# Kernel optimization log

Hardware: AMD Instinct MI355X
Metric: run time of the kernel (lower is better)

Reference implementation:

```python
import jax, jax.numpy as jnp
import numpy as np

N, E, D, EDIM = 50000, 800000, 128, 1
LN_EPS = 1e-5
NORM_FACTOR = 1.0


def _ln(x, g, b):
    m = jnp.mean(x, axis=-1, keepdims=True)
    v = jnp.var(x, axis=-1, keepdims=True)
    return (x - m) * jax.lax.rsqrt(v + LN_EPS) * g + b


def _mlp(x, w1, b1, g, be, w2, b2):
    # Linear -> SiLU -> LayerNorm -> Linear (matches nn.Sequential in msg_net/out_net)
    h = jax.nn.silu(x @ w1 + b1)
    h = _ln(h, g, be)
    return h @ w2 + b2


def setup_inputs() -> dict:
    key = jax.random.key(0)
    ks = jax.random.split(key, 24)
    s = 1.0 / np.sqrt(D)
    sa = 1.0 / np.sqrt(2 * D + EDIM)
    f32 = jnp.float32
    return {
        "h": jax.random.normal(ks[0], (N, D), f32),
        "edge_attr": jax.random.uniform(ks[1], (E, EDIM), f32),
        "row": jax.random.randint(ks[2], (E,), 0, N),
        "col": jax.random.randint(ks[3], (E,), 0, N),
        "node_mask": jnp.ones((N, 1), f32),
        "edge_mask": jnp.ones((E, 1), f32),
        "lin_w": jax.random.normal(ks[4], (D, D), f32) * s,
        "lin_b": jnp.zeros((D,), f32),
        "msg_w1": jax.random.normal(ks[5], (D, D), f32) * s,
        "msg_b1": jnp.zeros((D,), f32),
        "msg_ln_g": jnp.ones((D,), f32),
        "msg_ln_b": jnp.zeros((D,), f32),
        "msg_w2": jax.random.normal(ks[6], (D, D), f32) * s,
        "msg_b2": jnp.zeros((D,), f32),
        "att_w1": jax.random.normal(ks[7], (2 * D + EDIM, D), f32) * sa,
        "att_b1": jnp.zeros((D,), f32),
        "att_w2": jax.random.normal(ks[8], (D, 1), f32) * s,
        "att_b2": jnp.zeros((1,), f32),
        "out_w1": jax.random.normal(ks[9], (D, D), f32) * s,
        "out_b1": jnp.zeros((D,), f32),
        "out_ln_g": jnp.ones((D,), f32),
        "out_ln_b": jnp.zeros((D,), f32),
        "out_w2": jax.random.normal(ks[10], (D, D), f32) * s,
        "out_b2": jnp.zeros((D,), f32),
        "ln_g": jnp.ones((D,), f32),
        "ln_b": jnp.zeros((D,), f32),
    }


def reference(h, edge_attr, row, col, node_mask, edge_mask,
              lin_w, lin_b,
              msg_w1, msg_b1, msg_ln_g, msg_ln_b, msg_w2, msg_b2,
              att_w1, att_b1, att_w2, att_b2,
              out_w1, out_b1, out_ln_g, out_ln_b, out_w2, out_b2,
              ln_g, ln_b):
    # h = self.linear(h)
    x = h @ lin_w + lin_b                                    # [N, D]
    # msg_net transform of node features
    x_ = _mlp(x, msg_w1, msg_b1, msg_ln_g, msg_ln_b, msg_w2, msg_b2)
    # DenseAtt: cat(x[row], x[col], edge_attr) -> MLP -> sigmoid -> * edge_mask
    feat = jnp.concatenate([x[row], x[col], edge_attr], axis=1)   # [E, 2D+edge_dim]
    att = jax.nn.sigmoid(jax.nn.silu(feat @ att_w1 + att_b1) @ att_w2 + att_b2)
    att = att * edge_mask                                    # [E, 1]
    # gather -> weighted message -> scatter_add (unsorted_segment_sum, 'sum' norm)
    msg = jax.ops.segment_sum(x_[col] * att, row, num_segments=N) / NORM_FACTOR
    # out_net transform, residual, final LayerNorm
    msg = _mlp(msg, out_w1, out_b1, out_ln_g, out_ln_b, out_w2, out_b2)
    return _ln(x + msg, ln_g, ln_b)                          # [N, D]
```

## Files before the change

### kernel.cpp

```cpp
#include <hip/hip_runtime.h>

#define LN_EPS 1e-5f

typedef __attribute__((ext_vector_type(8))) short short8;
typedef __attribute__((ext_vector_type(4))) float f32x4;

__device__ __forceinline__ float sigf(float x) {
    return __builtin_amdgcn_rcpf(1.0f + __expf(-x));
}

__device__ __forceinline__ unsigned short f2bf(float f) {
    unsigned u = __float_as_uint(f);
    return (unsigned short)((u + 0x7fffu + ((u >> 16) & 1u)) >> 16);
}
__device__ __forceinline__ unsigned f2bf2(float lo, float hi) {
    return (unsigned)f2bf(lo) | ((unsigned)f2bf(hi) << 16);
}
__device__ __forceinline__ void bf2f(unsigned u, float& lo, float& hi) {
    lo = __uint_as_float(u << 16);
    hi = __uint_as_float(u & 0xffff0000u);
}
__device__ __forceinline__ void bf8f(uint4 p, float* o) {
    bf2f(p.x, o[0], o[1]); bf2f(p.y, o[2], o[3]);
    bf2f(p.z, o[4], o[5]); bf2f(p.w, o[6], o[7]);
}
__device__ __forceinline__ float bf1f(unsigned short s) {
    return __uint_as_float(((unsigned)s) << 16);
}

__device__ __forceinline__ float quad_add_all(float x) {
    int v = __builtin_amdgcn_update_dpp(0, __float_as_int(x), 0xB1, 0xF, 0xF, true);
    x += __int_as_float(v);
    v = __builtin_amdgcn_update_dpp(0, __float_as_int(x), 0x4E, 0xF, 0xF, true);
    x += __int_as_float(v);
    return x;
}

__global__ __launch_bounds__(256)
void prep_w(const float* __restrict__ lin_w, const float* __restrict__ msg_w1,
            const float* __restrict__ msg_w2, const float* __restrict__ att_w1,
            const float* __restrict__ out_w1, const float* __restrict__ out_w2,
            const float* __restrict__ att_b1, unsigned short* __restrict__ wp,
            float* __restrict__ bias256)
{
    const int idx = blockIdx.x * 256 + threadIdx.x;
    if (idx < 8 * 16384) {
        const int m = idx >> 14, r = idx & 16383;
        const int k = r >> 7, n = r & 127;
        const float* src; int slot; int fnBase = 0;
        switch (m) {
            case 0: src = lin_w;  slot = 0; break;
            case 1: src = msg_w1; slot = 1; break;
            case 2: src = msg_w2; slot = 2; break;
            case 3: src = att_w1; slot = 3; break;
            case 4: src = att_w1 + 128 * 128; slot = 3; fnBase = 8; break;
            case 5: src = out_w1; slot = 5; break;
            default: src = out_w2; slot = 6; break;
        }
        const float v = src[k * 128 + n];
        const int fn = fnBase + (n >> 4);
        const int fk = k >> 5, kb = (k >> 3) & 3, j = k & 7;
        const size_t dst = (size_t)slot * 16384 + ((size_t)((fn * 4 + fk) * 64 + (n & 15) + 16 * kb)) * 8 + j;
        wp[dst] = f2bf(v);
    } else if (idx < 8 * 16384 + 256) {
        const int t = idx - 8 * 16384;
        bias256[t] = (t < 128) ? att_b1[t] : 0.f;
    }
}

__device__ __forceinline__ short8 ldA_f32(const float* A, size_t row, int k0) {
    const float* ap = A + row * 128 + k0;
    const float4 f0 = *(const float4*)ap;
    const float4 f1 = *(const float4*)(ap + 4);
    union { unsigned u[4]; short8 s; } v;
    v.u[0] = f2bf2(f0.x, f0.y); v.u[1] = f2bf2(f0.z, f0.w);
    v.u[2] = f2bf2(f1.x, f1.y); v.u[3] = f2bf2(f1.z, f1.w);
    return v.s;
}
__device__ __forceinline__ short8 ldA_bf(const unsigned short* A, size_t row, int k0) {
    return *(const short8*)(A + row * 128 + k0);
}

__global__ __launch_bounds__(256, 4)
void front_mfma(const float* __restrict__ h,
                const unsigned short* __restrict__ WpLin, const float* __restrict__ lin_b,
                const unsigned short* __restrict__ WpAtt, const float* __restrict__ bias256,
                const unsigned short* __restrict__ WpM1, const float* __restrict__ msg_b1,
                const float* __restrict__ m1g, const float* __restrict__ m1b,
                const unsigned short* __restrict__ WpM2, const float* __restrict__ msg_b2,
                unsigned short* __restrict__ xbH, unsigned short* __restrict__ xrH,
                unsigned short* __restrict__ xcH, unsigned short* __restrict__ xmH,
                int nrows)
{
    __shared__ unsigned short hofA[4 * 2048];
    __shared__ unsigned short hofB[4 * 2048];
    const int tid = threadIdx.x;
    const int w = tid >> 6, lane = tid & 63;
    const int r0 = blockIdx.x * 64;
    const int arow = r0 + w * 16 + (lane & 15);
    const size_t rowc = (arow < nrows) ? (size_t)arow : (size_t)(nrows - 1);
    const int kh = (lane >> 4) * 8;
    const int cn = lane & 15, rq = lane >> 4;
    unsigned short* hwA = hofA + w * 2048;
    unsigned short* hwB = hofB + w * 2048;

    short8 a[4];
#pragma unroll
    for (int fk = 0; fk < 4; ++fk) a[fk] = ldA_f32(h, rowc, fk * 32 + kh);

    {
        const short8* Bf = (const short8*)WpLin;
        f32x4 accx[8];
#pragma unroll
        for (int fn = 0; fn < 8; ++fn) accx[fn] = (f32x4){0.f, 0.f, 0.f, 0.f};
#pragma unroll
        for (int fk = 0; fk < 4; ++fk)
#pragma unroll
            for (int fn = 0; fn < 8; ++fn)
                accx[fn] = __builtin_amdgcn_mfma_f32_16x16x32_bf16(a[fk], Bf[(fn * 4 + fk) * 64 + lane], accx[fn], 0, 0, 0);

        float bv[8];
#pragma unroll
        for (int fn = 0; fn < 8; ++fn) bv[fn] = lin_b[fn * 16 + cn];
#pragma unroll
        for (int reg = 0; reg < 4; ++reg) {
            const int gr = r0 + w * 16 + rq * 4 + reg;
            const int row16 = rq * 4 + reg;
            const int sw = (row16 & 7) << 3;
#pragma unroll
            for (int fn = 0; fn < 8; ++fn) {
                const unsigned short hb = f2bf(accx[fn][reg] + bv[fn]);
                if (gr < nrows) xbH[(size_t)gr * 128 + fn * 16 + cn] = hb;
                hwA[row16 * 128 + ((fn * 16 + cn) ^ sw)] = hb;
            }
        }
    }

    short8 ax[4];
    {
        const int row16 = lane & 15;
        const int sw = (row16 & 7) << 3;
#pragma unroll
        for (int fk = 0; fk < 4; ++fk)
            ax[fk] = *(const short8*)(hwA + row16 * 128 + ((fk * 32 + kh) ^ sw));
    }

    {
        const short8* Bf = (const short8*)WpAtt;
        f32x4 acca[16];
#pragma unroll
        for (int fn = 0; fn < 16; ++fn) acca[fn] = (f32x4){0.f, 0.f, 0.f, 0.f};
#pragma unroll
        for (int fk = 0; fk < 4; ++fk)
#pragma unroll
            for (int fn = 0; fn < 16; ++fn)
                acca[fn] = __builtin_amdgcn_mfma_f32_16x16x32_bf16(ax[fk], Bf[(fn * 4 + fk) * 64 + lane], acca[fn], 0, 0, 0);

        float bv[16];
#pragma unroll
        for (int fn = 0; fn < 16; ++fn) bv[fn] = bias256[fn * 16 + cn];
#pragma unroll
        for (int reg = 0; reg < 4; ++reg) {
            const int gr = r0 + w * 16 + rq * 4 + reg;
            if (gr < nrows) {
#pragma unroll
                for (int fn = 0; fn < 16; ++fn) {
                    const float v = acca[fn][reg] + bv[fn];
                    if (fn < 8) xrH[(size_t)gr * 128 + fn * 16 + cn] = f2bf(v);
                    else        xcH[(size_t)gr * 128 + (fn - 8) * 16 + cn] = f2bf(v);
                }
            }
        }
    }

    {
        const short8* Bf = (const short8*)WpM1;
        f32x4 acc1[8];
#pragma unroll
        for (int fn = 0; fn < 8; ++fn) acc1[fn] = (f32x4){0.f, 0.f, 0.f, 0.f};
#pragma unroll
        for (int fk = 0; fk < 4; ++fk)
#pragma unroll
            for (int fn = 0; fn < 8; ++fn)
                acc1[fn] = __builtin_amdgcn_mfma_f32_16x16x32_bf16(ax[fk], Bf[(fn * 4 + fk) * 64 + lane], acc1[fn], 0, 0, 0);

        float bv[8], gv[8], bbv[8];
#pragma unroll
        for (int fn = 0; fn < 8; ++fn) {
            bv[fn] = msg_b1[fn * 16 + cn]; gv[fn] = m1g[fn * 16 + cn]; bbv[fn] = m1b[fn * 16 + cn];
        }
#pragma unroll
        for (int reg = 0; reg < 4; ++reg) {
            float val[8];
            float sum = 0.f, sq = 0.f;
#pragma unroll
            for (int fn = 0; fn < 8; ++fn) {
                float v = acc1[fn][reg] + bv[fn];
                v = v * sigf(v);
                val[fn] = v; sum += v; sq += v * v;
            }
#pragma unroll
            for (int m = 1; m < 16; m <<= 1) { sum += __shfl_xor(sum, m); sq += __shfl_xor(sq, m); }
            const float mean = sum * (1.f / 128.f);
            const float var = sq * (1.f / 128.f) - mean * mean;
            const float rstd = rsqrtf(var + LN_EPS);
            const int row16 = rq * 4 + reg;
            const int sw = (row16 & 7) << 3;
#pragma unroll
            for (int fn = 0; fn < 8; ++fn) {
                const float o = (val[fn] - mean) * rstd * gv[fn] + bbv[fn];
                hwB[row16 * 128 + ((fn * 16 + cn) ^ sw)] = f2bf(o);
            }
        }
    }

    short8 am[4];
    {
        const int row16 = lane & 15;
        const int sw = (row16 & 7) << 3;
#pragma unroll
        for (int fk = 0; fk < 4; ++fk)
            am[fk] = *(const short8*)(hwB + row16 * 128 + ((fk * 32 + kh) ^ sw));
    }
    {
        const short8* Bf = (const short8*)WpM2;
        f32x4 acc2[8];
#pragma unroll
        for (int fn = 0; fn < 8; ++fn) acc2[fn] = (f32x4){0.f, 0.f, 0.f, 0.f};
#pragma unroll
        for (int fk = 0; fk < 4; ++fk)
#pragma unroll
            for (int fn = 0; fn < 8; ++fn)
                acc2[fn] = __builtin_amdgcn_mfma_f32_16x16x32_bf16(am[fk], Bf[(fn * 4 + fk) * 64 + lane], acc2[fn], 0, 0, 0);

        float bv[8];
#pragma unroll
        for (int fn = 0; fn < 8; ++fn) bv[fn] = msg_b2[fn * 16 + cn];
#pragma unroll
        for (int reg = 0; reg < 4; ++reg) {
            const int gr = r0 + w * 16 + rq * 4 + reg;
            if (gr < nrows) {
#pragma unroll
                for (int fn = 0; fn < 8; ++fn)
                    xmH[(size_t)gr * 128 + fn * 16 + cn] = f2bf(acc2[fn][reg] + bv[fn]);
            }
        }
    }
}

__global__ __launch_bounds__(256, 4)
void gemm2_mfma(const unsigned short* __restrict__ Av,
                const unsigned short* __restrict__ Wp1, const float* __restrict__ b1,
                const float* __restrict__ ln1g, const float* __restrict__ ln1b,
                const unsigned short* __restrict__ Wp2, const float* __restrict__ b2,
                const float* __restrict__ ln2g, const float* __restrict__ ln2b,
                const unsigned short* __restrict__ resH, float* __restrict__ Cf, int nrows)
{
    __shared__ unsigned short hof[4 * 2048];
    const int tid = threadIdx.x;
    const int w = tid >> 6, lane = tid & 63;
    const int r0 = blockIdx.x * 64;
    const int arow = r0 + w * 16 + (lane & 15);
    const size_t rowc = (arow < nrows) ? (size_t)arow : (size_t)(nrows - 1);
    const int kh = (lane >> 4) * 8;
    const int cn = lane & 15, rq = lane >> 4;

    short8 a[4];
#pragma unroll
    for (int fk = 0; fk < 4; ++fk) a[fk] = ldA_bf(Av, rowc, fk * 32 + kh);

    const short8* B1f = (const short8*)Wp1;
    f32x4 acc[8];
#pragma unroll
    for (int fn = 0; fn < 8; ++fn) acc[fn] = (f32x4){0.f, 0.f, 0.f, 0.f};
#pragma unroll
    for (int fk = 0; fk < 4; ++fk)
#pragma unroll
        for (int fn = 0; fn < 8; ++fn)
            acc[fn] = __builtin_amdgcn_mfma_f32_16x16x32_bf16(a[fk], B1f[(fn * 4 + fk) * 64 + lane], acc[fn], 0, 0, 0);

    unsigned short* hw = hof + w * 2048;
    {
        float bv[8], gv[8], bbv[8];
#pragma unroll
        for (int fn = 0; fn < 8; ++fn) {
            bv[fn] = b1[fn * 16 + cn]; gv[fn] = ln1g[fn * 16 + cn]; bbv[fn] = ln1b[fn * 16 + cn];
        }
#pragma unroll
        for (int reg = 0; reg < 4; ++reg) {
            float val[8];
            float sum = 0.f, sq = 0.f;
#pragma unroll
            for (int fn = 0; fn < 8; ++fn) {
                float v = acc[fn][reg] + bv[fn];
                v = v * sigf(v);
                val[fn] = v; sum += v; sq += v * v;
            }
#pragma unroll
            for (int m = 1; m < 16; m <<= 1) { sum += __shfl_xor(sum, m); sq += __shfl_xor(sq, m); }
            const float mean = sum * (1.f / 128.f);
            const float var = sq * (1.f / 128.f) - mean * mean;
            const float rstd = rsqrtf(var + LN_EPS);
            const int row16 = rq * 4 + reg;
            const int sw = (row16 & 7) << 3;
#pragma unroll
            for (int fn = 0; fn < 8; ++fn) {
                const float o = (val[fn] - mean) * rstd * gv[fn] + bbv[fn];
                hw[row16 * 128 + ((fn * 16 + cn) ^ sw)] = f2bf(o);
            }
        }
    }

    short8 a2[4];
    {
        const int row16 = lane & 15;
        const int sw = (row16 & 7) << 3;
#pragma unroll
        for (int fk = 0; fk < 4; ++fk)
            a2[fk] = *(const short8*)(hw + row16 * 128 + ((fk * 32 + kh) ^ sw));
    }

    const short8* B2f = (const short8*)Wp2;
    f32x4 acc2[8];
#pragma unroll
    for (int fn = 0; fn < 8; ++fn) acc2[fn] = (f32x4){0.f, 0.f, 0.f, 0.f};
#pragma unroll
    for (int fk = 0; fk < 4; ++fk)
#pragma unroll
        for (int fn = 0; fn < 8; ++fn)
            acc2[fn] = __builtin_amdgcn_mfma_f32_16x16x32_bf16(a2[fk], B2f[(fn * 4 + fk) * 64 + lane], acc2[fn], 0, 0, 0);

    float bv2[8], gv[8], bbv[8];
#pragma unroll
    for (int fn = 0; fn < 8; ++fn) {
        bv2[fn] = b2[fn * 16 + cn]; gv[fn] = ln2g[fn * 16 + cn]; bbv[fn] = ln2b[fn * 16 + cn];
    }
#pragma unroll
    for (int reg = 0; reg < 4; ++reg) {
        const int gr = r0 + w * 16 + rq * 4 + reg;
        const int grc = gr < nrows ? gr : nrows - 1;
        float val[8];
        float sum = 0.f, sq = 0.f;
#pragma unroll
        for (int fn = 0; fn < 8; ++fn) {
            float v = acc2[fn][reg] + bv2[fn] + bf1f(resH[(size_t)grc * 128 + fn * 16 + cn]);
            val[fn] = v; sum += v; sq += v * v;
        }
#pragma unroll
        for (int m = 1; m < 16; m <<= 1) { sum += __shfl_xor(sum, m); sq += __shfl_xor(sq, m); }
        const float mean = sum * (1.f / 128.f);
        const float var = sq * (1.f / 128.f) - mean * mean;
        const float rstd = rsqrtf(var + LN_EPS);
        if (gr < nrows) {
#pragma unroll
            for (int fn = 0; fn < 8; ++fn)
                Cf[(size_t)gr * 128 + fn * 16 + cn] = (val[fn] - mean) * rstd * gv[fn] + bbv[fn];
        }
    }
}

__global__ __launch_bounds__(256)
void hist_rank(const int* __restrict__ row, int* __restrict__ cnt,
               int* __restrict__ rank, int E)
{
    const int tid = blockIdx.x * blockDim.x + threadIdx.x;
    const int stride = gridDim.x * blockDim.x;
    for (int e0 = tid; e0 < E; e0 += stride * 8) {
        int r[8]; bool val[8];
#pragma unroll
        for (int u = 0; u < 8; ++u) {
            const int e = e0 + u * stride;
            val[u] = e < E;
            r[u] = val[u] ? row[e] : 0;
        }
        int rk[8];
#pragma unroll
        for (int u = 0; u < 8; ++u)
            if (val[u]) rk[u] = atomicAdd(&cnt[r[u]], 1);
#pragma unroll
        for (int u = 0; u < 8; ++u)
            if (val[u]) rank[e0 + u * stride] = rk[u];
    }
}

__global__ __launch_bounds__(1024)
void scan_a(const int* __restrict__ cnt, int* __restrict__ off,
            int* __restrict__ btot, int n)
{
    __shared__ int wsum[16];
    const int tid = threadIdx.x, lane = tid & 63, wv = tid >> 6;
    const int i = blockIdx.x * 1024 + tid;
    const int v = (i < n) ? cnt[i] : 0;
    int incl = v;
#pragma unroll
    for (int d = 1; d < 64; d <<= 1) { int t = __shfl_up(incl, d); if (lane >= d) incl += t; }
    if (lane == 63) wsum[wv] = incl;
    __syncthreads();
    if (tid == 0) {
        int run = 0;
        for (int ww = 0; ww < 16; ++ww) { int t = wsum[ww]; wsum[ww] = run; run += t; }
    }
    __syncthreads();
    if (i < n) off[i] = wsum[wv] + incl - v;
    if (tid == 1023) btot[blockIdx.x] = wsum[15] + incl;
}

__global__ __launch_bounds__(64)
void scan_b(int* __restrict__ btot, int* __restrict__ bexc,
            int* __restrict__ off, int n, int nb, int E)
{
    const int t = threadIdx.x;
    const int v = (t < nb) ? btot[t] : 0;
    int incl = v;
#pragma unroll
    for (int d = 1; d < 64; d <<= 1) { int u = __shfl_up(incl, d); if (t >= d) incl += u; }
    if (t < nb) bexc[t] = incl - v;
    if (t == 0) off[n] = E;
}

__global__ __launch_bounds__(1024)
void scan_c(int* __restrict__ off, const int* __restrict__ bexc, int n)
{
    const int i = blockIdx.x * 1024 + threadIdx.x;
    if (i < n) off[i] += bexc[blockIdx.x];
}

__global__ __launch_bounds__(256, 4)
void att_edge(const unsigned short* __restrict__ xrH,
              const unsigned short* __restrict__ xcH,
              const int* __restrict__ row, const int* __restrict__ col,
              const float* __restrict__ ea, const float* __restrict__ em,
              const int* __restrict__ rank, const int* __restrict__ off,
              const float* __restrict__ we_, const float* __restrict__ w2_,
              const float* __restrict__ b2p, uint2* __restrict__ catS, int E)
{
    const int lane = threadIdx.x & 63;
    const int q = lane & 3;
    const int gwid = (blockIdx.x * blockDim.x + threadIdx.x) >> 6;
    const int nw = (gridDim.x * blockDim.x) >> 6;

    float we[32], w2[32];
#pragma unroll
    for (int ch = 0; ch < 4; ++ch) {
        const float4 a0 = ((const float4*)we_)[ch * 8 + q * 2];
        const float4 a1 = ((const float4*)we_)[ch * 8 + q * 2 + 1];
        we[ch * 8 + 0] = a0.x; we[ch * 8 + 1] = a0.y; we[ch * 8 + 2] = a0.z; we[ch * 8 + 3] = a0.w;
        we[ch * 8 + 4] = a1.x; we[ch * 8 + 5] = a1.y; we[ch * 8 + 6] = a1.z; we[ch * 8 + 7] = a1.w;
        const float4 c0 = ((const float4*)w2_)[ch * 8 + q * 2];
        const float4 c1 = ((const float4*)w2_)[ch * 8 + q * 2 + 1];
        w2[ch * 8 + 0] = c0.x; w2[ch * 8 + 1] = c0.y; w2[ch * 8 + 2] = c0.z; w2[ch * 8 + 3] = c0.w;
        w2[ch * 8 + 4] = c1.x; w2[ch * 8 + 5] = c1.y; w2[ch * 8 + 6] = c1.z; w2[ch * 8 + 7] = c1.w;
    }
    const float b2 = *b2p;

    for (int base = gwid * 16; base < E; base += nw * 16) {
        const int e = base + (lane >> 2);
        const bool valid = e < E;
        const int ec = valid ? e : E - 1;
        const int r = row[ec], c = col[ec];
        const float eax = ea[ec], emv = em[ec];
        const unsigned short* xr = xrH + (size_t)r * 128;
        const unsigned short* xc = xcH + (size_t)c * 128;
        float pc[4];
#pragma unroll
        for (int ch = 0; ch < 4; ++ch) {
            const uint4 pa = *(const uint4*)(xr + ch * 32 + q * 8);
            const uint4 pb = *(const uint4*)(xc + ch * 32 + q * 8);
            float xa[8], xb[8];
            bf8f(pa, xa); bf8f(pb, xb);
            float s = 0.f;
#pragma unroll
            for (int i = 0; i < 8; ++i) {
                const float t = xa[i] + xb[i] + eax * we[ch * 8 + i];
                s += t * sigf(t) * w2[ch * 8 + i];
            }
            pc[ch] = s;
        }
        float p = (pc[0] + pc[1]) + (pc[2] + pc[3]);
        p = quad_add_all(p);
        const float att = sigf(p + b2) * emv;
        if (valid && q == 0) {
            const int pos = off[r] + rank[ec];
            catS[pos] = make_uint2((unsigned)c, __float_as_uint(att));
        }
    }
}

__global__ __launch_bounds__(256)
void accum_k(const unsigned short* __restrict__ xmH, const int* __restrict__ off,
             const uint2* __restrict__ catS, unsigned short* __restrict__ msgH, int N)
{
    const int lane = threadIdx.x & 63;
    const int g = lane >> 4, l = lane & 15;
    const int gwid = (blockIdx.x * blockDim.x + threadIdx.x) >> 6;
    const int nw = (gridDim.x * blockDim.x) >> 6;
    const uint4* xm4 = (const uint4*)xmH;

    for (int wid = gwid; wid < N; wid += nw) {
        int j0 = off[wid];
        const int jend = off[wid + 1];
        float acc[8] = {0.f, 0.f, 0.f, 0.f, 0.f, 0.f, 0.f, 0.f};

        for (; j0 + 16 <= jend; j0 += 16) {
            uint2 ca[4]; uint4 pk[4];
#pragma unroll
            for (int u = 0; u < 4; ++u) ca[u] = catS[j0 + u * 4 + g];
#pragma unroll
            for (int u = 0; u < 4; ++u) pk[u] = xm4[(size_t)ca[u].x * 16 + l];
#pragma unroll
            for (int u = 0; u < 4; ++u) {
                const float att = __uint_as_float(ca[u].y);
                float xm[8];
                bf8f(pk[u], xm);
#pragma unroll
                for (int i = 0; i < 8; ++i) acc[i] = fmaf(att, xm[i], acc[i]);
            }
        }
        for (; j0 + 8 <= jend; j0 += 8) {
            const uint2 caA = catS[j0 + g];
            const uint2 caB = catS[j0 + 4 + g];
            const uint4 pA = xm4[(size_t)caA.x * 16 + l];
            const uint4 pB = xm4[(size_t)caB.x * 16 + l];
            const float attA = __uint_as_float(caA.y);
            const float attB = __uint_as_float(caB.y);
            float xmA[8], xmB[8];
            bf8f(pA, xmA); bf8f(pB, xmB);
#pragma unroll
            for (int i = 0; i < 8; ++i)
                acc[i] = fmaf(attB, xmB[i], fmaf(attA, xmA[i], acc[i]));
        }
        for (; j0 < jend; j0 += 4) {
            const int je = j0 + g;
            const bool valid = je < jend;
            const int jc = valid ? je : jend - 1;
            const uint2 ca = catS[jc];
            const uint4 p = xm4[(size_t)ca.x * 16 + l];
            const float att = valid ? __uint_as_float(ca.y) : 0.f;
            float xm[8];
            bf8f(p, xm);
#pragma unroll
            for (int i = 0; i < 8; ++i) acc[i] = fmaf(att, xm[i], acc[i]);
        }

#pragma unroll
        for (int i = 0; i < 8; ++i) {
            acc[i] += __shfl_xor(acc[i], 16);
            acc[i] += __shfl_xor(acc[i], 32);
        }
        if (g == 0) {
            uint4 pk;
            pk.x = f2bf2(acc[0], acc[1]); pk.y = f2bf2(acc[2], acc[3]);
            pk.z = f2bf2(acc[4], acc[5]); pk.w = f2bf2(acc[6], acc[7]);
            ((uint4*)msgH)[(size_t)wid * 16 + l] = pk;
        }
    }
}

extern "C" void kernel_launch(void* const* d_in, const int* in_sizes, int n_in,
                              void* d_out, int out_size, void* d_ws, size_t ws_size,
                              hipStream_t stream)
{
    const float* h        = (const float*)d_in[0];
    const float* edge_attr= (const float*)d_in[1];
    const int*   row      = (const int*)d_in[2];
    const int*   col      = (const int*)d_in[3];
    const float* edge_mask= (const float*)d_in[5];
    const float* lin_w    = (const float*)d_in[6];
    const float* lin_b    = (const float*)d_in[7];
    const float* msg_w1   = (const float*)d_in[8];
    const float* msg_b1   = (const float*)d_in[9];
    const float* msg_ln_g = (const float*)d_in[10];
    const float* msg_ln_b = (const float*)d_in[11];
    const float* msg_w2   = (const float*)d_in[12];
    const float* msg_b2   = (const float*)d_in[13];
    const float* att_w1   = (const float*)d_in[14];
    const float* att_b1   = (const float*)d_in[15];
    const float* att_w2   = (const float*)d_in[16];
    const float* att_b2   = (const float*)d_in[17];
    const float* out_w1   = (const float*)d_in[18];
    const float* out_b1   = (const float*)d_in[19];
    const float* out_ln_g = (const float*)d_in[20];
    const float* out_ln_b = (const float*)d_in[21];
    const float* out_w2   = (const float*)d_in[22];
    const float* out_b2   = (const float*)d_in[23];
    const float* ln_g     = (const float*)d_in[24];
    const float* ln_b     = (const float*)d_in[25];

    const int N = in_sizes[0] / 128;
    const int E = in_sizes[2];
    const size_t NF = (size_t)N * 128;

    unsigned short* xbH  = (unsigned short*)d_ws;
    unsigned short* xrH  = xbH + NF;
    unsigned short* xcH  = xrH + NF;
    unsigned short* xmH  = xcH + NF;
    unsigned short* msgH = xmH + NF;
    int*    cnt   = (int*)(msgH + NF);
    int*    off   = cnt + N;
    int*    btot  = off + N + 8;
    int*    bexc  = btot + 64;
    int*    rank  = bexc + 64;
    uint2*  catS  = (uint2*)(rank + E);
    unsigned short* wp = (unsigned short*)(catS + E);
    float* bias256 = (float*)(wp + 8 * 16384);

    const int gb = (N + 63) / 64;
    const int nb = (N + 1023) / 1024;
    const int hgrid = (E + 256 * 8 - 1) / (256 * 8);

    prep_w<<<513, 256, 0, stream>>>(lin_w, msg_w1, msg_w2, att_w1, out_w1, out_w2,
                                    att_b1, wp, bias256);
    hipMemsetAsync(cnt, 0, (size_t)N * sizeof(int), stream);
    hist_rank<<<hgrid, 256, 0, stream>>>(row, cnt, rank, E);
    scan_a<<<nb, 1024, 0, stream>>>(cnt, off, btot, N);
    scan_b<<<1, 64, 0, stream>>>(btot, bexc, off, N, nb, E);
    scan_c<<<nb, 1024, 0, stream>>>(off, bexc, N);

    front_mfma<<<gb, 256, 0, stream>>>(h, wp, lin_b,
                                       wp + 3 * 16384, bias256,
                                       wp + 16384, msg_b1, msg_ln_g, msg_ln_b,
                                       wp + 2 * 16384, msg_b2,
                                       xbH, xrH, xcH, xmH, N);

    att_edge<<<2048, 256, 0, stream>>>(xrH, xcH, row, col, edge_attr, edge_mask,
                                       rank, off, att_w1 + 256 * 128, att_w2, att_b2,
                                       catS, E);

    accum_k<<<2048, 256, 0, stream>>>(xmH, off, catS, msgH, N);

    gemm2_mfma<<<gb, 256, 0, stream>>>(msgH, wp + 5 * 16384, out_b1, out_ln_g, out_ln_b,
                                       wp + 6 * 16384, out_b2, ln_g, ln_b,
                                       xbH, (float*)d_out, N);
}
```

Baseline: 230.9 us.

## Stage front_mfma weights in LDS and coalesce output stores via shared tiles

The front kernel now copies each 128x128 bf16 weight slab into a 32KB shared buffer before its MFMA pass, so B fragments come from LDS instead of repeated global/L2 reads. The fused 256-wide attention GEMM is split into two 128-wide passes. All outputs go through a swizzled LDS tile and are written as 16-byte vector stores rather than scattered 2-byte stores. In exchange the kernel adds several block barriers and more LDS use, and launch bounds drop to 3 blocks per CU.

```diff
diff --git a/kernel.cpp b/kernel.cpp
--- a/kernel.cpp
+++ b/kernel.cpp
@@ -81,19 +81,19 @@
     return *(const short8*)(A + row * 128 + k0);
 }
 
-__global__ __launch_bounds__(256, 4)
+__global__ __launch_bounds__(256, 3)
 void front_mfma(const float* __restrict__ h,
-                const unsigned short* __restrict__ WpLin, const float* __restrict__ lin_b,
-                const unsigned short* __restrict__ WpAtt, const float* __restrict__ bias256,
-                const unsigned short* __restrict__ WpM1, const float* __restrict__ msg_b1,
+                const unsigned short* __restrict__ wp, const float* __restrict__ lin_b,
+                const float* __restrict__ att_b1,
+                const float* __restrict__ msg_b1,
                 const float* __restrict__ m1g, const float* __restrict__ m1b,
-                const unsigned short* __restrict__ WpM2, const float* __restrict__ msg_b2,
+                const float* __restrict__ msg_b2,
                 unsigned short* __restrict__ xbH, unsigned short* __restrict__ xrH,
                 unsigned short* __restrict__ xcH, unsigned short* __restrict__ xmH,
                 int nrows)
 {
-    __shared__ unsigned short hofA[4 * 2048];
-    __shared__ unsigned short hofB[4 * 2048];
+    __shared__ uint4 Bbuf[2048];
+    __shared__ unsigned short hof[4 * 2048];
     const int tid = threadIdx.x;
     const int w = tid >> 6, lane = tid & 63;
     const int r0 = blockIdx.x * 64;
@@ -101,89 +101,93 @@
     const size_t rowc = (arow < nrows) ? (size_t)arow : (size_t)(nrows - 1);
     const int kh = (lane >> 4) * 8;
     const int cn = lane & 15, rq = lane >> 4;
-    unsigned short* hwA = hofA + w * 2048;
-    unsigned short* hwB = hofB + w * 2048;
+    unsigned short* hw = hof + w * 2048;
+    const short8* Bf = (const short8*)Bbuf;
 
     short8 a[4];
 #pragma unroll
     for (int fk = 0; fk < 4; ++fk) a[fk] = ldA_f32(h, rowc, fk * 32 + kh);
 
-    {
-        const short8* Bf = (const short8*)WpLin;
-        f32x4 accx[8];
-#pragma unroll
-        for (int fn = 0; fn < 8; ++fn) accx[fn] = (f32x4){0.f, 0.f, 0.f, 0.f};
-#pragma unroll
-        for (int fk = 0; fk < 4; ++fk)
-#pragma unroll
-            for (int fn = 0; fn < 8; ++fn)
-                accx[fn] = __builtin_amdgcn_mfma_f32_16x16x32_bf16(a[fk], Bf[(fn * 4 + fk) * 64 + lane], accx[fn], 0, 0, 0);
-
+    const uint4* wp4 = (const uint4*)wp;
+
+#define LOADB(slotoff)  { _Pragma("unroll") \
+    for (int i = 0; i < 8; ++i) Bbuf[tid + i * 256] = wp4[(slotoff) + tid + i * 256]; }
+
+#define MFMA8(afrag, accv) { _Pragma("unroll") \
+    for (int fk = 0; fk < 4; ++fk) { _Pragma("unroll") \
+        for (int fn = 0; fn < 8; ++fn) \
+            accv[fn] = __builtin_amdgcn_mfma_f32_16x16x32_bf16(afrag[fk], Bf[(fn * 4 + fk) * 64 + lane], accv[fn], 0, 0, 0); } }
+
+#define EPI_HOF(accv, bvv) { _Pragma("unroll") \
+    for (int reg = 0; reg < 4; ++reg) { \
+        const int row16 = rq * 4 + reg; const int sw = (row16 & 7) << 3; _Pragma("unroll") \
+        for (int fn = 0; fn < 8; ++fn) \
+            hw[row16 * 128 + ((fn * 16 + cn) ^ sw)] = f2bf(accv[fn][reg] + bvv[fn]); } }
+
+#define FLUSH(G) { const int frow = lane >> 2; const int fgr = r0 + w * 16 + frow; \
+    const int fsw = (frow & 7) << 3; _Pragma("unroll") \
+    for (int it = 0; it < 4; ++it) { \
+        const int c0 = ((lane & 3) + it * 4) * 8; \
+        short8 v = *(const short8*)(hw + frow * 128 + (c0 ^ fsw)); \
+        if (fgr < nrows) *(short8*)((G) + (size_t)fgr * 128 + c0) = v; } }
+
+    LOADB(0);
+    __syncthreads();
+    f32x4 acc[8];
+#pragma unroll
+    for (int fn = 0; fn < 8; ++fn) acc[fn] = (f32x4){0.f, 0.f, 0.f, 0.f};
+    MFMA8(a, acc);
+    {
         float bv[8];
 #pragma unroll
         for (int fn = 0; fn < 8; ++fn) bv[fn] = lin_b[fn * 16 + cn];
-#pragma unroll
-        for (int reg = 0; reg < 4; ++reg) {
-            const int gr = r0 + w * 16 + rq * 4 + reg;
-            const int row16 = rq * 4 + reg;
-            const int sw = (row16 & 7) << 3;
-#pragma unroll
-            for (int fn = 0; fn < 8; ++fn) {
-                const unsigned short hb = f2bf(accx[fn][reg] + bv[fn]);
-                if (gr < nrows) xbH[(size_t)gr * 128 + fn * 16 + cn] = hb;
-                hwA[row16 * 128 + ((fn * 16 + cn) ^ sw)] = hb;
-            }
-        }
-    }
-
+        EPI_HOF(acc, bv);
+    }
     short8 ax[4];
     {
         const int row16 = lane & 15;
         const int sw = (row16 & 7) << 3;
 #pragma unroll
         for (int fk = 0; fk < 4; ++fk)
-            ax[fk] = *(const short8*)(hwA + row16 * 128 + ((fk * 32 + kh) ^ sw));
-    }
-
-    {
-        const short8* Bf = (const short8*)WpAtt;
-        f32x4 acca[16];
-#pragma unroll
-        for (int fn = 0; fn < 16; ++fn) acca[fn] = (f32x4){0.f, 0.f, 0.f, 0.f};
-#pragma unroll
-        for (int fk = 0; fk < 4; ++fk)
-#pragma unroll
-            for (int fn = 0; fn < 16; ++fn)
-                acca[fn] = __builtin_amdgcn_mfma_f32_16x16x32_bf16(ax[fk], Bf[(fn * 4 + fk) * 64 + lane], acca[fn], 0, 0, 0);
-
-        float bv[16];
-#pragma unroll
-        for (int fn = 0; fn < 16; ++fn) bv[fn] = bias256[fn * 16 + cn];
-#pragma unroll
-        for (int reg = 0; reg < 4; ++reg) {
-            const int gr = r0 + w * 16 + rq * 4 + reg;
-            if (gr < nrows) {
-#pragma unroll
-                for (int fn = 0; fn < 16; ++fn) {
-                    const float v = acca[fn][reg] + bv[fn];
-                    if (fn < 8) xrH[(size_t)gr * 128 + fn * 16 + cn] = f2bf(v);
-                    else        xcH[(size_t)gr * 128 + (fn - 8) * 16 + cn] = f2bf(v);
-                }
-            }
-        }
-    }
-
-    {
-        const short8* Bf = (const short8*)WpM1;
-        f32x4 acc1[8];
-#pragma unroll
-        for (int fn = 0; fn < 8; ++fn) acc1[fn] = (f32x4){0.f, 0.f, 0.f, 0.f};
-#pragma unroll
-        for (int fk = 0; fk < 4; ++fk)
-#pragma unroll
-            for (int fn = 0; fn < 8; ++fn)
-                acc1[fn] = __builtin_amdgcn_mfma_f32_16x16x32_bf16(ax[fk], Bf[(fn * 4 + fk) * 64 + lane], acc1[fn], 0, 0, 0);
-
+            ax[fk] = *(const short8*)(hw + row16 * 128 + ((fk * 32 + kh) ^ sw));
+    }
+    FLUSH(xbH);
+    __syncthreads();
+
+    LOADB(3 * 2048);
+    __syncthreads();
+#pragma unroll
+    for (int fn = 0; fn < 8; ++fn) acc[fn] = (f32x4){0.f, 0.f, 0.f, 0.f};
+    MFMA8(ax, acc);
+    {
+        float bv[8];
+#pragma unroll
+        for (int fn = 0; fn < 8; ++fn) bv[fn] = att_b1[fn * 16 + cn];
+        EPI_HOF(acc, bv);
+    }
+    FLUSH(xrH);
+    __syncthreads();
+
+    LOADB(4 * 2048);
+    __syncthreads();
+#pragma unroll
+    for (int fn = 0; fn < 8; ++fn) acc[fn] = (f32x4){0.f, 0.f, 0.f, 0.f};
+    MFMA8(ax, acc);
+    {
+        float bv[8];
+#pragma unroll
+        for (int fn = 0; fn < 8; ++fn) bv[fn] = 0.f;
+        EPI_HOF(acc, bv);
+    }
+    FLUSH(xcH);
+    __syncthreads();
+
+    LOADB(1 * 2048);
+    __syncthreads();
+#pragma unroll
+    for (int fn = 0; fn < 8; ++fn) acc[fn] = (f32x4){0.f, 0.f, 0.f, 0.f};
+    MFMA8(ax, acc);
+    {
         float bv[8], gv[8], bbv[8];
 #pragma unroll
         for (int fn = 0; fn < 8; ++fn) {
@@ -195,7 +199,7 @@
             float sum = 0.f, sq = 0.f;
 #pragma unroll
             for (int fn = 0; fn < 8; ++fn) {
-                float v = acc1[fn][reg] + bv[fn];
+                float v = acc[fn][reg] + bv[fn];
                 v = v * sigf(v);
                 val[fn] = v; sum += v; sq += v * v;
             }
@@ -209,43 +213,36 @@
 #pragma unroll
             for (int fn = 0; fn < 8; ++fn) {
                 const float o = (val[fn] - mean) * rstd * gv[fn] + bbv[fn];
-                hwB[row16 * 128 + ((fn * 16 + cn) ^ sw)] = f2bf(o);
+                hw[row16 * 128 + ((fn * 16 + cn) ^ sw)] = f2bf(o);
             }
         }
     }
-
     short8 am[4];
     {
         const int row16 = lane & 15;
         const int sw = (row16 & 7) << 3;
 #pragma unroll
         for (int fk = 0; fk < 4; ++fk)
-            am[fk] = *(const short8*)(hwB + row16 * 128 + ((fk * 32 + kh) ^ sw));
-    }
-    {
-        const short8* Bf = (const short8*)WpM2;
-        f32x4 acc2[8];
-#pragma unroll
-        for (int fn = 0; fn < 8; ++fn) acc2[fn] = (f32x4){0.f, 0.f, 0.f, 0.f};
-#pragma unroll
-        for (int fk = 0; fk < 4; ++fk)
-#pragma unroll
-            for (int fn = 0; fn < 8; ++fn)
-                acc2[fn] = __builtin_amdgcn_mfma_f32_16x16x32_bf16(am[fk], Bf[(fn * 4 + fk) * 64 + lane], acc2[fn], 0, 0, 0);
-
+            am[fk] = *(const short8*)(hw + row16 * 128 + ((fk * 32 + kh) ^ sw));
+    }
+    __syncthreads();
+
+    LOADB(2 * 2048);
+    __syncthreads();
+#pragma unroll
+    for (int fn = 0; fn < 8; ++fn) acc[fn] = (f32x4){0.f, 0.f, 0.f, 0.f};
+    MFMA8(am, acc);
+    {
         float bv[8];
 #pragma unroll
         for (int fn = 0; fn < 8; ++fn) bv[fn] = msg_b2[fn * 16 + cn];
-#pragma unroll
-        for (int reg = 0; reg < 4; ++reg) {
-            const int gr = r0 + w * 16 + rq * 4 + reg;
-            if (gr < nrows) {
-#pragma unroll
-                for (int fn = 0; fn < 8; ++fn)
-                    xmH[(size_t)gr * 128 + fn * 16 + cn] = f2bf(acc2[fn][reg] + bv[fn]);
-            }
-        }
-    }
+        EPI_HOF(acc, bv);
+    }
+    FLUSH(xmH);
+#undef LOADB
+#undef MFMA8
+#undef EPI_HOF
+#undef FLUSH
 }
 
 __global__ __launch_bounds__(256, 4)
@@ -616,10 +613,8 @@
     scan_b<<<1, 64, 0, stream>>>(btot, bexc, off, N, nb, E);
     scan_c<<<nb, 1024, 0, stream>>>(off, bexc, N);
 
-    front_mfma<<<gb, 256, 0, stream>>>(h, wp, lin_b,
-                                       wp + 3 * 16384, bias256,
-                                       wp + 16384, msg_b1, msg_ln_g, msg_ln_b,
-                                       wp + 2 * 16384, msg_b2,
+    front_mfma<<<gb, 256, 0, stream>>>(h, wp, lin_b, att_b1,
+                                       msg_b1, msg_ln_g, msg_ln_b, msg_b2,
                                        xbH, xrH, xcH, xmH, N);
 
     att_edge<<<2048, 256, 0, stream>>>(xrH, xcH, row, col, edge_attr, edge_mask,
```

After: 201.9 us. 1.14x faster.
